# Optimization experiments

Hardware: AMD Instinct MI355X
Metric: run time of the kernel (lower is better)

The kernel has to match this reference:

```python
import jax, jax.numpy as jnp
import numpy as np

B, H, S, D = 2, 16, 2048, 64

def setup_inputs() -> dict:
    key = jax.random.key(0)
    kq, kk, kv = jax.random.split(key, 3)
    Q = jax.random.normal(kq, (B, H, S, D), dtype=jnp.float32)
    K = jax.random.normal(kk, (B, H, S, D), dtype=jnp.float32)
    V = jax.random.normal(kv, (B, H, S, D), dtype=jnp.float32)
    # causal mask: True means 'masked out' (filled with -inf), as in torch.masked_fill
    mask = jnp.triu(jnp.ones((S, S), dtype=bool), k=1)[None, None, :, :]
    return {"Q": Q, "K": K, "V": V, "mask": mask}

def reference(Q, K, V, mask):
    head_dim = jnp.asarray(K.shape[-1], dtype=Q.dtype)
    # a_scaled = Q @ K^T / sqrt(d)   -> [B,H,S,S]
    scores = jnp.einsum('bhqd,bhkd->bhqk', Q, K) / jnp.sqrt(head_dim)
    scores = jnp.where(mask, -jnp.inf, scores)
    # NOTE: the original custom softmax subtracts the GLOBAL max of the whole
    # tensor (torch.max(x) with no dim), not a per-row max. Reproduce faithfully.
    m = jnp.max(scores)
    e = jnp.exp(scores - m)
    attn = e / jnp.sum(e, axis=-1, keepdims=True)
    return jnp.einsum('bhqk,bhkd->bhqd', attn, V)
```

## Files before the change

kernel.cpp:

```cpp
#include <hip/hip_runtime.h>
#include <hip/hip_bf16.h>
#include <cstdint>
#include <cstddef>

#define SLEN 2048
#define DH   64
#define NQT  32
#define QBLK 64
#define KVB  64
#define NHEADS 32
#define LOG2E 1.44269504088896340736f

#define PRE_HEAD_BYTES (SLEN * DH * 2)
#define TILE_BYTES     (KVB * DH * 2)
#define VPRE_OFF       ((size_t)NHEADS * PRE_HEAD_BYTES)

typedef short  bf16x8 __attribute__((ext_vector_type(8)));
typedef float  f32x4  __attribute__((ext_vector_type(4)));

__device__ __forceinline__ unsigned short f2bf(float f) {
    __hip_bfloat16 h = __float2bfloat16(f);
    return *reinterpret_cast<unsigned short*>(&h);
}
__device__ __forceinline__ unsigned int pk2(float a, float b) {
    return (unsigned int)f2bf(a) | ((unsigned int)f2bf(b) << 16);
}

#define GLL(gp, lp)                                                            \
    __builtin_amdgcn_global_load_lds(                                          \
        (const __attribute__((address_space(1))) void*)(gp),                   \
        (__attribute__((address_space(3))) void*)(lp), 16, 0, 0)

__global__ __launch_bounds__(256) void prep(const float* __restrict__ Kg,
                                            const float* __restrict__ Vg,
                                            unsigned short* __restrict__ ws)
{
    const int bid = blockIdx.x;
    const int tid = threadIdx.x;
    if (bid < 2048) {
        const int cid = bid * 256 + tid;
        const int h   = cid >> 14;
        const int rem = cid & 16383;
        const int r   = rem >> 3;
        const int ccs = rem & 7;
        const int d0  = 8 * (ccs ^ (r & 7));
        const float* src = Kg + ((size_t)h * SLEN + r) * DH + d0;
        float4 a = *reinterpret_cast<const float4*>(src);
        float4 b = *reinterpret_cast<const float4*>(src + 4);
        bf16x8 o;
        o[0]=(short)f2bf(a.x); o[1]=(short)f2bf(a.y);
        o[2]=(short)f2bf(a.z); o[3]=(short)f2bf(a.w);
        o[4]=(short)f2bf(b.x); o[5]=(short)f2bf(b.y);
        o[6]=(short)f2bf(b.z); o[7]=(short)f2bf(b.w);
        *(bf16x8*)((char*)ws + (size_t)cid * 16) = o;
    } else {
        __shared__ __attribute__((aligned(16))) unsigned short Vt[KVB * DH];
        const int vb = bid - 2048;
        const int h  = vb >> 5;
        const int t  = vb & 31;
        const int do8 = tid & 7;
        const int kp  = tid >> 3;
        const float* s0 = Vg + ((size_t)h * SLEN + (size_t)t * KVB + 2 * kp) * DH + 8 * do8;
        float4 a0 = *reinterpret_cast<const float4*>(s0);
        float4 a1 = *reinterpret_cast<const float4*>(s0 + 4);
        float4 b0 = *reinterpret_cast<const float4*>(s0 + DH);
        float4 b1 = *reinterpret_cast<const float4*>(s0 + DH + 4);
        float av[8] = {a0.x,a0.y,a0.z,a0.w,a1.x,a1.y,a1.z,a1.w};
        float bv[8] = {b0.x,b0.y,b0.z,b0.w,b1.x,b1.y,b1.z,b1.w};
        #pragma unroll
        for (int j = 0; j < 8; ++j) {
            const int d = 8 * do8 + j;
            const unsigned byte =
                ((unsigned)(d * 128 + 4 * kp)) ^ (((unsigned)(d & 7)) << 4);
            *(unsigned*)((char*)Vt + byte) = pk2(av[j], bv[j]);
        }
        __syncthreads();
        char* gdst = (char*)ws + VPRE_OFF + (size_t)h * PRE_HEAD_BYTES
                   + (size_t)t * TILE_BYTES + (size_t)tid * 32;
        const char* lsrc = (const char*)Vt + tid * 32;
        *(bf16x8*)(gdst)      = *(const bf16x8*)(lsrc);
        *(bf16x8*)(gdst + 16) = *(const bf16x8*)(lsrc + 16);
    }
}

__global__ __launch_bounds__(256, 4) void fattn_f(const float* __restrict__ Qg,
                                                  const unsigned short* __restrict__ KV,
                                                  float* __restrict__ Og)
{
    __shared__ __attribute__((aligned(16))) unsigned short Klds[2][KVB * DH];
    __shared__ __attribute__((aligned(16))) unsigned short Vlds[2][DH * KVB];
    __shared__ __attribute__((aligned(16))) unsigned short Plds[4][16 * KVB];

    const int bid = blockIdx.x;
    const int hi4 = bid >> 8;
    const int lo8 = bid & 255;
    const int qx  = (int)((0x0F101F00u >> (8 * hi4)) & 31u);
    const int qt  = (lo8 & 31) ^ qx;
    const int bh  = (hi4 << 3) | (lo8 >> 5);
    const int qb  = qt * QBLK;

    const float* Qp   = Qg + (size_t)bh * SLEN * DH;
    const char*  Kpre = (const char*)KV + (size_t)bh * PRE_HEAD_BYTES;
    const char*  Vpre = (const char*)KV + VPRE_OFF + (size_t)bh * PRE_HEAD_BYTES;
    float*       Op   = Og + (size_t)bh * SLEN * DH;

    const int tid  = threadIdx.x;
    const int w    = tid >> 6;
    const int lane = tid & 63;
    const int g    = lane >> 4;
    const int m    = lane & 15;

    bf16x8 qf[2];
    {
        const float sc = 0.125f * LOG2E;
        const int qrow = qb + 16 * w + m;
        #pragma unroll
        for (int c = 0; c < 2; ++c) {
            const float* src = Qp + (size_t)qrow * DH + 32 * c + 8 * g;
            float4 a = *reinterpret_cast<const float4*>(src);
            float4 b = *reinterpret_cast<const float4*>(src + 4);
            bf16x8 qv;
            qv[0]=(short)f2bf(a.x*sc); qv[1]=(short)f2bf(a.y*sc);
            qv[2]=(short)f2bf(a.z*sc); qv[3]=(short)f2bf(a.w*sc);
            qv[4]=(short)f2bf(b.x*sc); qv[5]=(short)f2bf(b.y*sc);
            qv[6]=(short)f2bf(b.z*sc); qv[7]=(short)f2bf(b.w*sc);
            qf[c] = qv;
        }
    }

    f32x4 o[4];
    #pragma unroll
    for (int dt = 0; dt < 4; ++dt) o[dt] = (f32x4){0.f, 0.f, 0.f, 0.f};
    float mrun = -1e30f, lrun = 0.f;

    const int nt = qt + 1;

    char* Pw = (char*)&Plds[w][0];
    const unsigned pswz = ((unsigned)(m & 7)) << 4;
    const int q = qb + 16 * w + m;

    #define STAGE(jt_, buf_)                                                   \
        do {                                                                   \
            const char* gk_ = Kpre + (size_t)(jt_) * TILE_BYTES + tid * 16;    \
            const char* gv_ = Vpre + (size_t)(jt_) * TILE_BYTES + tid * 16;    \
            char* lk_ = (char*)&Klds[buf_][0] + tid * 16;                      \
            char* lv_ = (char*)&Vlds[buf_][0] + tid * 16;                      \
            GLL(gk_,        lk_);                                              \
            GLL(gk_ + 4096, lk_ + 4096);                                       \
            GLL(gv_,        lv_);                                              \
            GLL(gv_ + 4096, lv_ + 4096);                                       \
        } while (0)

    int buf = 0;
    STAGE(0, 0);
    __syncthreads();

    for (int jt = 0; jt < nt; ++jt) {
        const int kvb   = jt * KVB;
        const bool last = (jt == nt - 1);

        if (jt + 1 < nt) STAGE(jt + 1, buf ^ 1);

        const char* Kb = (const char*)&Klds[buf][0];
        const char* Vb = (const char*)&Vlds[buf][0];

        f32x4 s[4];
        #pragma unroll
        for (int t = 0; t < 4; ++t) {
            s[t] = (f32x4){0.f, 0.f, 0.f, 0.f};
            #pragma unroll
            for (int c = 0; c < 2; ++c) {
                const unsigned row  = (unsigned)(16 * t + m);
                const unsigned byte =
                    (row * 128u + (unsigned)(32 * c + 8 * g) * 2u) ^ ((row & 7u) << 4);
                bf16x8 kf = *(const bf16x8*)(Kb + byte);
                s[t] = __builtin_amdgcn_mfma_f32_16x16x32_bf16(kf, qf[c], s[t], 0, 0, 0);
            }
        }

        float mx = -1e30f;
        #pragma unroll
        for (int t = 0; t < 4; ++t) {
            #pragma unroll
            for (int r = 0; r < 4; ++r) {
                float v = s[t][r];
                if (last) {
                    const int kk = kvb + 16 * t + 4 * g + r;
                    v = (kk > q) ? -1e30f : v;
                }
                s[t][r] = v;
                mx = fmaxf(mx, v);
            }
        }
        mx = fmaxf(mx, __shfl_xor(mx, 16));
        mx = fmaxf(mx, __shfl_xor(mx, 32));
        const float mnew = fmaxf(mrun, mx);
        const float fs   = exp2f(mrun - mnew);
        mrun = mnew;

        float psum = 0.f;
        #pragma unroll
        for (int t = 0; t < 4; ++t) {
            const float p0 = exp2f(s[t][0] - mnew);
            const float p1 = exp2f(s[t][1] - mnew);
            const float p2 = exp2f(s[t][2] - mnew);
            const float p3 = exp2f(s[t][3] - mnew);
            psum += (p0 + p1) + (p2 + p3);
            uint2 e;
            e.x = pk2(p0, p1);
            e.y = pk2(p2, p3);
            const unsigned byte = (unsigned)(m * 128 + 32 * t + 8 * g);
            *(uint2*)(Pw + (byte ^ pswz)) = e;
        }
        psum += __shfl_xor(psum, 16);
        psum += __shfl_xor(psum, 32);
        lrun = lrun * fs + psum;

        float fso[4];
        #pragma unroll
        for (int r = 0; r < 4; ++r)
            fso[r] = __shfl(fs, (lane & 48) | (4 * g + r));
        #pragma unroll
        for (int dt = 0; dt < 4; ++dt) {
            #pragma unroll
            for (int r = 0; r < 4; ++r) o[dt][r] *= fso[r];
        }

        #pragma unroll
        for (int kc = 0; kc < 2; ++kc) {
            const unsigned ab = ((unsigned)(m * 128 + 64 * kc + 16 * g)) ^ pswz;
            bf16x8 pa = *(const bf16x8*)(Pw + ab);
            #pragma unroll
            for (int dt = 0; dt < 4; ++dt) {
                const unsigned d  = (unsigned)(16 * dt + m);
                const unsigned vby =
                    (d * 128u + (unsigned)(64 * kc + 16 * g)) ^ ((d & 7u) << 4);
                bf16x8 vf = *(const bf16x8*)(Vb + vby);
                o[dt] = __builtin_amdgcn_mfma_f32_16x16x32_bf16(pa, vf, o[dt], 0, 0, 0);
            }
        }

        __syncthreads();
        buf ^= 1;
    }
    #undef STAGE

    const float invl = 1.0f / lrun;
    float invo[4];
    #pragma unroll
    for (int r = 0; r < 4; ++r)
        invo[r] = __shfl(invl, (lane & 48) | (4 * g + r));
    #pragma unroll
    for (int r = 0; r < 4; ++r) {
        const int qrow = qb + 16 * w + 4 * g + r;
        float* dst = Op + (size_t)qrow * DH;
        #pragma unroll
        for (int dt = 0; dt < 4; ++dt) dst[16 * dt + m] = o[dt][r] * invo[r];
    }
}

__global__ __launch_bounds__(256, 4) void fattn_s(const float* __restrict__ Qg,
                                                  const float* __restrict__ Kg,
                                                  const float* __restrict__ Vg,
                                                  float* __restrict__ Og)
{
    __shared__ __attribute__((aligned(16))) unsigned short Klds[128 * DH];
    __shared__ __attribute__((aligned(16))) unsigned short Vlds[DH * 128];
    __shared__ __attribute__((aligned(16))) unsigned short Plds[4][16 * 128];

    const int bid = blockIdx.x;
    const int hi4 = bid >> 8;
    const int lo8 = bid & 255;
    const int qx  = (int)((0x0F101F00u >> (8 * hi4)) & 31u);
    const int qt  = (lo8 & 31) ^ qx;
    const int bh  = (hi4 << 3) | (lo8 >> 5);
    const int qb  = qt * QBLK;

    const float* Qp = Qg + (size_t)bh * SLEN * DH;
    const float* Kp = Kg + (size_t)bh * SLEN * DH;
    const float* Vp = Vg + (size_t)bh * SLEN * DH;
    float*       Op = Og + (size_t)bh * SLEN * DH;

    const int tid  = threadIdx.x;
    const int w    = tid >> 6;
    const int lane = tid & 63;
    const int g    = lane >> 4;
    const int m    = lane & 15;

    bf16x8 qf[2];
    {
        const float sc = 0.125f * LOG2E;
        const int qrow = qb + 16 * w + m;
        #pragma unroll
        for (int c = 0; c < 2; ++c) {
            const float* src = Qp + (size_t)qrow * DH + 32 * c + 8 * g;
            float4 a = *reinterpret_cast<const float4*>(src);
            float4 b = *reinterpret_cast<const float4*>(src + 4);
            bf16x8 qv;
            qv[0]=(short)f2bf(a.x*sc); qv[1]=(short)f2bf(a.y*sc);
            qv[2]=(short)f2bf(a.z*sc); qv[3]=(short)f2bf(a.w*sc);
            qv[4]=(short)f2bf(b.x*sc); qv[5]=(short)f2bf(b.y*sc);
            qv[6]=(short)f2bf(b.z*sc); qv[7]=(short)f2bf(b.w*sc);
            qf[c] = qv;
        }
    }

    f32x4 o[4];
    #pragma unroll
    for (int dt = 0; dt < 4; ++dt) o[dt] = (f32x4){0.f, 0.f, 0.f, 0.f};
    float mrun = -1e30f, lrun = 0.f;

    const int klim = qb + QBLK;
    const int nt   = (qt + 2) >> 1;

    const int rk = tid & 127, hk = tid >> 7;
    const int kp = tid & 63,  dq = tid >> 6;

    char* Pw = (char*)&Plds[w][0];
    const unsigned pswz = ((unsigned)(m & 7)) << 4;
    const int q = qb + 16 * w + m;

    for (int jt = 0; jt < nt; ++jt) {
        const int kvb    = jt * 128;
        const int kwidth = min(128, klim - kvb);
        const bool last  = (jt == nt - 1);

        if (rk < kwidth) {
            const float4* s4 = reinterpret_cast<const float4*>(
                Kp + (size_t)(kvb + rk) * DH + 32 * hk);
            float4 x[8];
            #pragma unroll
            for (int i = 0; i < 8; ++i) x[i] = s4[i];
            const unsigned rswz = ((unsigned)(rk & 7)) << 4;
            #pragma unroll
            for (int c = 0; c < 4; ++c) {
                bf16x8 kb;
                kb[0]=(short)f2bf(x[2*c].x);   kb[1]=(short)f2bf(x[2*c].y);
                kb[2]=(short)f2bf(x[2*c].z);   kb[3]=(short)f2bf(x[2*c].w);
                kb[4]=(short)f2bf(x[2*c+1].x); kb[5]=(short)f2bf(x[2*c+1].y);
                kb[6]=(short)f2bf(x[2*c+1].z); kb[7]=(short)f2bf(x[2*c+1].w);
                const unsigned byte = (unsigned)(rk * 128 + 64 * hk + 16 * c);
                *(bf16x8*)((char*)Klds + (byte ^ rswz)) = kb;
            }
        }
        if (2 * kp < kwidth) {
            const float* s0 = Vp + (size_t)(kvb + 2 * kp) * DH + 16 * dq;
            float av[16], bv[16];
            #pragma unroll
            for (int i = 0; i < 4; ++i) {
                float4 ta = *reinterpret_cast<const float4*>(s0 + 4 * i);
                float4 tb = *reinterpret_cast<const float4*>(s0 + DH + 4 * i);
                av[4*i]=ta.x; av[4*i+1]=ta.y; av[4*i+2]=ta.z; av[4*i+3]=ta.w;
                bv[4*i]=tb.x; bv[4*i+1]=tb.y; bv[4*i+2]=tb.z; bv[4*i+3]=tb.w;
            }
            #pragma unroll
            for (int j = 0; j < 16; ++j) {
                const int d = 16 * dq + j;
                const unsigned byte = (unsigned)(d * 256 + 4 * kp);
                *(unsigned*)((char*)Vlds + (byte ^ (((unsigned)(d & 7)) << 4))) =
                    pk2(av[j], bv[j]);
            }
        }
        __syncthreads();

        f32x4 s[8];
        #pragma unroll
        for (int t = 0; t < 8; ++t) {
            if (16 * t < kwidth) {
                s[t] = (f32x4){0.f, 0.f, 0.f, 0.f};
                #pragma unroll
                for (int c = 0; c < 2; ++c) {
                    const unsigned row  = (unsigned)(16 * t + m);
                    const unsigned byte =
                        (row * 128u + (unsigned)(32 * c + 8 * g) * 2u) ^ ((row & 7u) << 4);
                    bf16x8 kf = *(const bf16x8*)((const char*)Klds + byte);
                    s[t] = __builtin_amdgcn_mfma_f32_16x16x32_bf16(kf, qf[c], s[t], 0, 0, 0);
                }
            }
        }

        float mx = -1e30f;
        #pragma unroll
        for (int t = 0; t < 8; ++t) {
            if (16 * t < kwidth) {
                #pragma unroll
                for (int r = 0; r < 4; ++r) {
                    float v = s[t][r];
                    if (last) {
                        const int kk = kvb + 16 * t + 4 * g + r;
                        v = (kk > q) ? -1e30f : v;
                    }
                    s[t][r] = v;
                    mx = fmaxf(mx, v);
                }
            }
        }
        mx = fmaxf(mx, __shfl_xor(mx, 16));
        mx = fmaxf(mx, __shfl_xor(mx, 32));
        const float mnew = fmaxf(mrun, mx);
        const float fs   = exp2f(mrun - mnew);
        mrun = mnew;

        float psum = 0.f;
        #pragma unroll
        for (int t = 0; t < 8; ++t) {
            if (16 * t < kwidth) {
                const float p0 = exp2f(s[t][0] - mnew);
                const float p1 = exp2f(s[t][1] - mnew);
                const float p2 = exp2f(s[t][2] - mnew);
                const float p3 = exp2f(s[t][3] - mnew);
                psum += (p0 + p1) + (p2 + p3);
                uint2 e;
                e.x = pk2(p0, p1);
                e.y = pk2(p2, p3);
                const unsigned byte = (unsigned)(m * 256 + 32 * t + 8 * g);
                *(uint2*)(Pw + (byte ^ pswz)) = e;
            }
        }
        psum += __shfl_xor(psum, 16);
        psum += __shfl_xor(psum, 32);
        lrun = lrun * fs + psum;

        float fso[4];
        #pragma unroll
        for (int r = 0; r < 4; ++r)
            fso[r] = __shfl(fs, (lane & 48) | (4 * g + r));
        #pragma unroll
        for (int dt = 0; dt < 4; ++dt) {
            #pragma unroll
            for (int r = 0; r < 4; ++r) o[dt][r] *= fso[r];
        }

        const int kclim = kwidth >> 5;
        #pragma unroll
        for (int kc = 0; kc < 4; ++kc) {
            if (kc < kclim) {
                const unsigned ab = ((unsigned)(m * 256 + 64 * kc + 16 * g)) ^ pswz;
                bf16x8 pa = *(const bf16x8*)(Pw + ab);
                #pragma unroll
                for (int dt = 0; dt < 4; ++dt) {
                    const unsigned d  = (unsigned)(16 * dt + m);
                    const unsigned vby =
                        (d * 256u + (unsigned)(64 * kc + 16 * g)) ^ ((d & 7u) << 4);
                    bf16x8 vf = *(const bf16x8*)((const char*)Vlds + vby);
                    o[dt] = __builtin_amdgcn_mfma_f32_16x16x32_bf16(pa, vf, o[dt], 0, 0, 0);
                }
            }
        }
        __syncthreads();
    }

    const float invl = 1.0f / lrun;
    float invo[4];
    #pragma unroll
    for (int r = 0; r < 4; ++r)
        invo[r] = __shfl(invl, (lane & 48) | (4 * g + r));
    #pragma unroll
    for (int r = 0; r < 4; ++r) {
        const int qrow = qb + 16 * w + 4 * g + r;
        float* dst = Op + (size_t)qrow * DH;
        #pragma unroll
        for (int dt = 0; dt < 4; ++dt) dst[16 * dt + m] = o[dt][r] * invo[r];
    }
}

extern "C" void kernel_launch(void* const* d_in, const int* in_sizes, int n_in,
                              void* d_out, int out_size, void* d_ws, size_t ws_size,
                              hipStream_t stream) {
    const float* Q = (const float*)d_in[0];
    const float* K = (const float*)d_in[1];
    const float* V = (const float*)d_in[2];
    float* O = (float*)d_out;
    if (ws_size >= 2 * VPRE_OFF) {
        unsigned short* ws = (unsigned short*)d_ws;
        prep<<<dim3(3072), dim3(256), 0, stream>>>(K, V, ws);
        fattn_f<<<dim3(1024), dim3(256), 0, stream>>>(Q, ws, O);
    } else {
        fattn_s<<<dim3(1024), dim3(256), 0, stream>>>(Q, K, V, O);
    }
}
```

Before: 158.2 us.

## Triple-buffer KV tiles with manual vmcnt waits, lazy rescale, and LPT block order

Moves the K/V staging from double to triple buffering, prefetching two tiles ahead and replacing __syncthreads with explicit s_waitcnt vmcnt plus s_barrier. The block-to-tile mapping changes to a longest-first order (heaviest causal q-tiles first) in place of the XOR swizzle. The online-softmax rescale of o and l is skipped when no lane's max grows, and s_setprio raises wave priority around the MFMA sections. The larger LDS footprint drops launch bounds from 4 to 2 blocks per CU, which lowers occupancy in exchange for deeper prefetch. The hand-written vmcnt counts assume a fixed number of outstanding loads per stage.

```diff
diff --git a/kernel.cpp b/kernel.cpp
--- a/kernel.cpp
+++ b/kernel.cpp
@@ -83,20 +83,17 @@
     }
 }
 
-__global__ __launch_bounds__(256, 4) void fattn_f(const float* __restrict__ Qg,
+__global__ __launch_bounds__(256, 2) void fattn_f(const float* __restrict__ Qg,
                                                   const unsigned short* __restrict__ KV,
                                                   float* __restrict__ Og)
 {
-    __shared__ __attribute__((aligned(16))) unsigned short Klds[2][KVB * DH];
-    __shared__ __attribute__((aligned(16))) unsigned short Vlds[2][DH * KVB];
+    __shared__ __attribute__((aligned(16))) unsigned short Klds[3][KVB * DH];
+    __shared__ __attribute__((aligned(16))) unsigned short Vlds[3][DH * KVB];
     __shared__ __attribute__((aligned(16))) unsigned short Plds[4][16 * KVB];
 
     const int bid = blockIdx.x;
-    const int hi4 = bid >> 8;
-    const int lo8 = bid & 255;
-    const int qx  = (int)((0x0F101F00u >> (8 * hi4)) & 31u);
-    const int qt  = (lo8 & 31) ^ qx;
-    const int bh  = (hi4 << 3) | (lo8 >> 5);
+    const int qt  = 31 - (bid >> 5);
+    const int bh  = bid & 31;
     const int qb  = qt * QBLK;
 
     const float* Qp   = Qg + (size_t)bh * SLEN * DH;
@@ -139,32 +136,40 @@
     const unsigned pswz = ((unsigned)(m & 7)) << 4;
     const int q = qb + 16 * w + m;
 
-    #define STAGE(jt_, buf_)                                                   \
+    #define STAGE(jt_, b_)                                                     \
         do {                                                                   \
             const char* gk_ = Kpre + (size_t)(jt_) * TILE_BYTES + tid * 16;    \
             const char* gv_ = Vpre + (size_t)(jt_) * TILE_BYTES + tid * 16;    \
-            char* lk_ = (char*)&Klds[buf_][0] + tid * 16;                      \
-            char* lv_ = (char*)&Vlds[buf_][0] + tid * 16;                      \
+            char* lk_ = (char*)Klds + (size_t)(b_) * TILE_BYTES + tid * 16;    \
+            char* lv_ = (char*)Vlds + (size_t)(b_) * TILE_BYTES + tid * 16;    \
             GLL(gk_,        lk_);                                              \
             GLL(gk_ + 4096, lk_ + 4096);                                       \
             GLL(gv_,        lv_);                                              \
             GLL(gv_ + 4096, lv_ + 4096);                                       \
         } while (0)
 
-    int buf = 0;
+    int c0 = 0, c1 = 1, c2 = 2;
     STAGE(0, 0);
-    __syncthreads();
+    if (nt > 1) {
+        STAGE(1, 1);
+        asm volatile("s_waitcnt vmcnt(4)" ::: "memory");
+    } else {
+        asm volatile("s_waitcnt vmcnt(0)" ::: "memory");
+    }
+    __builtin_amdgcn_s_barrier();
 
     for (int jt = 0; jt < nt; ++jt) {
         const int kvb   = jt * KVB;
         const bool last = (jt == nt - 1);
-
-        if (jt + 1 < nt) STAGE(jt + 1, buf ^ 1);
-
-        const char* Kb = (const char*)&Klds[buf][0];
-        const char* Vb = (const char*)&Vlds[buf][0];
+        const bool more = (jt + 2 < nt);
+
+        if (more) STAGE(jt + 2, c2);
+
+        const char* Kb = (const char*)Klds + (size_t)c0 * TILE_BYTES;
+        const char* Vb = (const char*)Vlds + (size_t)c0 * TILE_BYTES;
 
         f32x4 s[4];
+        __builtin_amdgcn_s_setprio(1);
         #pragma unroll
         for (int t = 0; t < 4; ++t) {
             s[t] = (f32x4){0.f, 0.f, 0.f, 0.f};
@@ -177,6 +182,7 @@
                 s[t] = __builtin_amdgcn_mfma_f32_16x16x32_bf16(kf, qf[c], s[t], 0, 0, 0);
             }
         }
+        __builtin_amdgcn_s_setprio(0);
 
         float mx = -1e30f;
         #pragma unroll
@@ -194,17 +200,30 @@
         }
         mx = fmaxf(mx, __shfl_xor(mx, 16));
         mx = fmaxf(mx, __shfl_xor(mx, 32));
-        const float mnew = fmaxf(mrun, mx);
-        const float fs   = exp2f(mrun - mnew);
-        mrun = mnew;
+
+        if (__any(mx > mrun)) {
+            const float mnew = fmaxf(mrun, mx);
+            const float fs   = exp2f(mrun - mnew);
+            mrun = mnew;
+            lrun *= fs;
+            float fso[4];
+            #pragma unroll
+            for (int r = 0; r < 4; ++r)
+                fso[r] = __shfl(fs, (lane & 48) | (4 * g + r));
+            #pragma unroll
+            for (int dt = 0; dt < 4; ++dt) {
+                #pragma unroll
+                for (int r = 0; r < 4; ++r) o[dt][r] *= fso[r];
+            }
+        }
 
         float psum = 0.f;
         #pragma unroll
         for (int t = 0; t < 4; ++t) {
-            const float p0 = exp2f(s[t][0] - mnew);
-            const float p1 = exp2f(s[t][1] - mnew);
-            const float p2 = exp2f(s[t][2] - mnew);
-            const float p3 = exp2f(s[t][3] - mnew);
+            const float p0 = exp2f(s[t][0] - mrun);
+            const float p1 = exp2f(s[t][1] - mrun);
+            const float p2 = exp2f(s[t][2] - mrun);
+            const float p3 = exp2f(s[t][3] - mrun);
             psum += (p0 + p1) + (p2 + p3);
             uint2 e;
             e.x = pk2(p0, p1);
@@ -214,18 +233,9 @@
         }
         psum += __shfl_xor(psum, 16);
         psum += __shfl_xor(psum, 32);
-        lrun = lrun * fs + psum;
-
-        float fso[4];
-        #pragma unroll
-        for (int r = 0; r < 4; ++r)
-            fso[r] = __shfl(fs, (lane & 48) | (4 * g + r));
-        #pragma unroll
-        for (int dt = 0; dt < 4; ++dt) {
-            #pragma unroll
-            for (int r = 0; r < 4; ++r) o[dt][r] *= fso[r];
-        }
-
+        lrun += psum;
+
+        __builtin_amdgcn_s_setprio(1);
         #pragma unroll
         for (int kc = 0; kc < 2; ++kc) {
             const unsigned ab = ((unsigned)(m * 128 + 64 * kc + 16 * g)) ^ pswz;
@@ -239,9 +249,13 @@
                 o[dt] = __builtin_amdgcn_mfma_f32_16x16x32_bf16(pa, vf, o[dt], 0, 0, 0);
             }
         }
-
-        __syncthreads();
-        buf ^= 1;
+        __builtin_amdgcn_s_setprio(0);
+
+        if (more) asm volatile("s_waitcnt vmcnt(4)" ::: "memory");
+        else      asm volatile("s_waitcnt vmcnt(0)" ::: "memory");
+        __builtin_amdgcn_s_barrier();
+
+        const int tswap = c0; c0 = c1; c1 = c2; c2 = tswap;
     }
     #undef STAGE
 
```

Result: faster. 153.9 us (-2.7%).

## Pre-swizzle K/V into MFMA fragment order and load directly into registers

Applied to the files above, without the earlier changes.

The prep kernel now writes K and V tiles in the exact per-lane MFMA fragment order, so the attention kernel loads K/V straight from global memory into registers instead of staging them through LDS with global_load_lds. The new kernel handles 128 query rows per block (32 per wave, two 16-row halves) across 512 blocks, uses per-wave causal tile counts with no block barriers, and skips the rescale when no row max increases. This removes LDS traffic and __syncthreads, but each wave now reads K/V from global or L2 on its own, and register pressure rises, with launch bounds lowered to 2 blocks per CU.

```diff
diff --git a/kernel.cpp b/kernel.cpp
--- a/kernel.cpp
+++ b/kernel.cpp
@@ -5,15 +5,12 @@
 
 #define SLEN 2048
 #define DH   64
-#define NQT  32
-#define QBLK 64
-#define KVB  64
 #define NHEADS 32
 #define LOG2E 1.44269504088896340736f
 
-#define PRE_HEAD_BYTES (SLEN * DH * 2)
-#define TILE_BYTES     (KVB * DH * 2)
-#define VPRE_OFF       ((size_t)NHEADS * PRE_HEAD_BYTES)
+#define PRE_TILE 16384
+#define PRE_HEAD (32 * PRE_TILE)
+#define PRE_TOTAL ((size_t)NHEADS * PRE_HEAD)
 
 typedef short  bf16x8 __attribute__((ext_vector_type(8)));
 typedef float  f32x4  __attribute__((ext_vector_type(4)));
@@ -25,11 +22,6 @@
 __device__ __forceinline__ unsigned int pk2(float a, float b) {
     return (unsigned int)f2bf(a) | ((unsigned int)f2bf(b) << 16);
 }
-
-#define GLL(gp, lp)                                                            \
-    __builtin_amdgcn_global_load_lds(                                          \
-        (const __attribute__((address_space(1))) void*)(gp),                   \
-        (__attribute__((address_space(3))) void*)(lp), 16, 0, 0)
 
 __global__ __launch_bounds__(256) void prep(const float* __restrict__ Kg,
                                             const float* __restrict__ Vg,
@@ -38,13 +30,16 @@
     const int bid = blockIdx.x;
     const int tid = threadIdx.x;
     if (bid < 2048) {
-        const int cid = bid * 256 + tid;
-        const int h   = cid >> 14;
-        const int rem = cid & 16383;
-        const int r   = rem >> 3;
-        const int ccs = rem & 7;
-        const int d0  = 8 * (ccs ^ (r & 7));
-        const float* src = Kg + ((size_t)h * SLEN + r) * DH + d0;
+        const int cid  = bid * 256 + tid;
+        const int h    = cid >> 14;
+        const int rem  = cid & 16383;
+        const int jt   = rem >> 9;
+        const int rem2 = rem & 511;
+        const int kci  = rem2 >> 6;
+        const int l    = rem2 & 63;
+        const int t = kci >> 1, c = kci & 1, g = l >> 4, m = l & 15;
+        const float* src =
+            Kg + ((size_t)h * SLEN + 64 * jt + 16 * t + m) * DH + 32 * c + 8 * g;
         float4 a = *reinterpret_cast<const float4*>(src);
         float4 b = *reinterpret_cast<const float4*>(src + 4);
         bf16x8 o;
@@ -52,15 +47,17 @@
         o[2]=(short)f2bf(a.z); o[3]=(short)f2bf(a.w);
         o[4]=(short)f2bf(b.x); o[5]=(short)f2bf(b.y);
         o[6]=(short)f2bf(b.z); o[7]=(short)f2bf(b.w);
-        *(bf16x8*)((char*)ws + (size_t)cid * 16) = o;
+        *(bf16x8*)((char*)ws + (size_t)h * PRE_HEAD + (size_t)jt * PRE_TILE
+                   + kci * 1024 + l * 16) = o;
     } else {
-        __shared__ __attribute__((aligned(16))) unsigned short Vt[KVB * DH];
+        __shared__ __attribute__((aligned(16))) unsigned short Vt[64 * 64];
         const int vb = bid - 2048;
         const int h  = vb >> 5;
-        const int t  = vb & 31;
+        const int jt = vb & 31;
+        const int kp  = tid >> 3;
         const int do8 = tid & 7;
-        const int kp  = tid >> 3;
-        const float* s0 = Vg + ((size_t)h * SLEN + (size_t)t * KVB + 2 * kp) * DH + 8 * do8;
+        const float* s0 =
+            Vg + ((size_t)h * SLEN + 64 * jt + 2 * kp) * DH + 8 * do8;
         float4 a0 = *reinterpret_cast<const float4*>(s0);
         float4 a1 = *reinterpret_cast<const float4*>(s0 + 4);
         float4 b0 = *reinterpret_cast<const float4*>(s0 + DH);
@@ -71,25 +68,211 @@
         for (int j = 0; j < 8; ++j) {
             const int d = 8 * do8 + j;
             const unsigned byte =
-                ((unsigned)(d * 128 + 4 * kp)) ^ (((unsigned)(d & 7)) << 4);
+                (unsigned)(d * 128) + ((((unsigned)(kp >> 2)) ^ (unsigned)(d & 7)) << 4)
+                + (unsigned)((kp & 3) * 4);
             *(unsigned*)((char*)Vt + byte) = pk2(av[j], bv[j]);
         }
         __syncthreads();
-        char* gdst = (char*)ws + VPRE_OFF + (size_t)h * PRE_HEAD_BYTES
-                   + (size_t)t * TILE_BYTES + (size_t)tid * 32;
-        const char* lsrc = (const char*)Vt + tid * 32;
-        *(bf16x8*)(gdst)      = *(const bf16x8*)(lsrc);
-        *(bf16x8*)(gdst + 16) = *(const bf16x8*)(lsrc + 16);
-    }
-}
-
-__global__ __launch_bounds__(256, 4) void fattn_f(const float* __restrict__ Qg,
+        char* base = (char*)ws + (size_t)h * PRE_HEAD + (size_t)jt * PRE_TILE + 8192;
+        #pragma unroll
+        for (int u = 0; u < 2; ++u) {
+            const int cc  = 2 * tid + u;
+            const int vci = cc >> 6;
+            const int l   = cc & 63;
+            const int kc = vci >> 2, dt = vci & 3, g = l >> 4, m = l & 15;
+            const int d   = 16 * dt + m;
+            const int kch = 4 * kc + g;
+            bf16x8 v = *(const bf16x8*)((const char*)Vt + d * 128
+                        + (((unsigned)kch ^ (unsigned)(d & 7)) << 4));
+            *(bf16x8*)(base + vci * 1024 + l * 16) = v;
+        }
+    }
+}
+
+__global__ __launch_bounds__(256, 2) void fattn_r(const float* __restrict__ Qg,
                                                   const unsigned short* __restrict__ KV,
                                                   float* __restrict__ Og)
 {
-    __shared__ __attribute__((aligned(16))) unsigned short Klds[2][KVB * DH];
-    __shared__ __attribute__((aligned(16))) unsigned short Vlds[2][DH * KVB];
-    __shared__ __attribute__((aligned(16))) unsigned short Plds[4][16 * KVB];
+    __shared__ __attribute__((aligned(16))) unsigned short Plds[4][2][16 * 64];
+
+    const int bid   = blockIdx.x;
+    const int hi    = bid >> 8;
+    const int qtile = (bid & 15) ^ (hi ? 15 : 0);
+    const int head  = (bid >> 4) & 31;
+    const int Qb    = qtile * 128;
+
+    const float* Qp = Qg + (size_t)head * SLEN * DH;
+    const char*  KH = (const char*)KV + (size_t)head * PRE_HEAD;
+    float*       Op = Og + (size_t)head * SLEN * DH;
+
+    const int tid  = threadIdx.x;
+    const int w    = tid >> 6;
+    const int lane = tid & 63;
+    const int g    = lane >> 4;
+    const int m    = lane & 15;
+
+    char* P0 = (char*)&Plds[w][0][0];
+    char* P1 = (char*)&Plds[w][1][0];
+    const unsigned pswz = ((unsigned)(m & 7)) << 4;
+
+    bf16x8 qf[2][2];
+    {
+        const float sc = 0.125f * LOG2E;
+        #pragma unroll
+        for (int h = 0; h < 2; ++h) {
+            const int qrow = Qb + 32 * w + 16 * h + m;
+            #pragma unroll
+            for (int c = 0; c < 2; ++c) {
+                const float* src = Qp + (size_t)qrow * DH + 32 * c + 8 * g;
+                float4 a = *reinterpret_cast<const float4*>(src);
+                float4 b = *reinterpret_cast<const float4*>(src + 4);
+                bf16x8 qv;
+                qv[0]=(short)f2bf(a.x*sc); qv[1]=(short)f2bf(a.y*sc);
+                qv[2]=(short)f2bf(a.z*sc); qv[3]=(short)f2bf(a.w*sc);
+                qv[4]=(short)f2bf(b.x*sc); qv[5]=(short)f2bf(b.y*sc);
+                qv[6]=(short)f2bf(b.z*sc); qv[7]=(short)f2bf(b.w*sc);
+                qf[h][c] = qv;
+            }
+        }
+    }
+
+    f32x4 o0[4], o1[4];
+    #pragma unroll
+    for (int dt = 0; dt < 4; ++dt) { o0[dt] = (f32x4){0,0,0,0}; o1[dt] = (f32x4){0,0,0,0}; }
+    float mr0 = -1e30f, lr0 = 0.f, mr1 = -1e30f, lr1 = 0.f;
+
+    const int q0 = Qb + 32 * w + m;
+    const int q1 = q0 + 16;
+    const int nt = 2 * qtile + 1 + (w >> 1);
+
+    const char* tb = KH;
+    for (int jt = 0; jt < nt; ++jt, tb += PRE_TILE) {
+        const bool last = (jt == nt - 1);
+        const int  kvb  = jt * 64;
+
+        bf16x8 kf[8];
+        #pragma unroll
+        for (int i = 0; i < 8; ++i)
+            kf[i] = *(const bf16x8*)(tb + i * 1024 + lane * 16);
+
+        f32x4 s0[4], s1[4];
+        #pragma unroll
+        for (int t = 0; t < 4; ++t) { s0[t] = (f32x4){0,0,0,0}; s1[t] = (f32x4){0,0,0,0}; }
+        #pragma unroll
+        for (int c = 0; c < 2; ++c) {
+            #pragma unroll
+            for (int t = 0; t < 4; ++t)
+                s0[t] = __builtin_amdgcn_mfma_f32_16x16x32_bf16(kf[2*t+c], qf[0][c], s0[t], 0, 0, 0);
+            #pragma unroll
+            for (int t = 0; t < 4; ++t)
+                s1[t] = __builtin_amdgcn_mfma_f32_16x16x32_bf16(kf[2*t+c], qf[1][c], s1[t], 0, 0, 0);
+        }
+
+        bf16x8 vf[8];
+        #pragma unroll
+        for (int i = 0; i < 8; ++i)
+            vf[i] = *(const bf16x8*)(tb + 8192 + i * 1024 + lane * 16);
+
+        #pragma unroll
+        for (int h = 0; h < 2; ++h) {
+            f32x4* s   = h ? s1 : s0;
+            float& mr  = h ? mr1 : mr0;
+            float& lr  = h ? lr1 : lr0;
+            f32x4* o   = h ? o1 : o0;
+            const int q = h ? q1 : q0;
+            char*  Pb  = h ? P1 : P0;
+
+            float mx = -1e30f;
+            #pragma unroll
+            for (int t = 0; t < 4; ++t) {
+                #pragma unroll
+                for (int r = 0; r < 4; ++r) {
+                    float v = s[t][r];
+                    if (last) {
+                        const int kk = kvb + 16 * t + 4 * g + r;
+                        v = (kk > q) ? -1e30f : v;
+                    }
+                    s[t][r] = v;
+                    mx = fmaxf(mx, v);
+                }
+            }
+            mx = fmaxf(mx, __shfl_xor(mx, 16));
+            mx = fmaxf(mx, __shfl_xor(mx, 32));
+
+            if (__any(mx > mr)) {
+                const float mnew = fmaxf(mr, mx);
+                const float fs   = exp2f(mr - mnew);
+                mr = mnew;
+                lr *= fs;
+                float fso[4];
+                #pragma unroll
+                for (int r = 0; r < 4; ++r)
+                    fso[r] = __shfl(fs, (lane & 48) | (4 * g + r));
+                #pragma unroll
+                for (int dt = 0; dt < 4; ++dt) {
+                    #pragma unroll
+                    for (int r = 0; r < 4; ++r) o[dt][r] *= fso[r];
+                }
+            }
+
+            float ps = 0.f;
+            #pragma unroll
+            for (int t = 0; t < 4; ++t) {
+                const float p0 = exp2f(s[t][0] - mr);
+                const float p1 = exp2f(s[t][1] - mr);
+                const float p2 = exp2f(s[t][2] - mr);
+                const float p3 = exp2f(s[t][3] - mr);
+                ps += (p0 + p1) + (p2 + p3);
+                uint2 e;
+                e.x = pk2(p0, p1);
+                e.y = pk2(p2, p3);
+                const unsigned byte = (unsigned)(m * 128 + 32 * t + 8 * g);
+                *(uint2*)(Pb + (byte ^ pswz)) = e;
+            }
+            ps += __shfl_xor(ps, 16);
+            ps += __shfl_xor(ps, 32);
+            lr += ps;
+        }
+
+        #pragma unroll
+        for (int kc = 0; kc < 2; ++kc) {
+            const unsigned ab = ((unsigned)(m * 128 + 64 * kc + 16 * g)) ^ pswz;
+            bf16x8 pa0 = *(const bf16x8*)(P0 + ab);
+            bf16x8 pa1 = *(const bf16x8*)(P1 + ab);
+            #pragma unroll
+            for (int dt = 0; dt < 4; ++dt) {
+                o0[dt] = __builtin_amdgcn_mfma_f32_16x16x32_bf16(pa0, vf[kc*4+dt], o0[dt], 0, 0, 0);
+                o1[dt] = __builtin_amdgcn_mfma_f32_16x16x32_bf16(pa1, vf[kc*4+dt], o1[dt], 0, 0, 0);
+            }
+        }
+    }
+
+    #pragma unroll
+    for (int h = 0; h < 2; ++h) {
+        const float invl = 1.0f / (h ? lr1 : lr0);
+        f32x4* o = h ? o1 : o0;
+        float invo[4];
+        #pragma unroll
+        for (int r = 0; r < 4; ++r)
+            invo[r] = __shfl(invl, (lane & 48) | (4 * g + r));
+        #pragma unroll
+        for (int r = 0; r < 4; ++r) {
+            const int qrow = Qb + 32 * w + 16 * h + 4 * g + r;
+            float* dst = Op + (size_t)qrow * DH;
+            #pragma unroll
+            for (int dt = 0; dt < 4; ++dt) dst[16 * dt + m] = o[dt][r] * invo[r];
+        }
+    }
+}
+
+__global__ __launch_bounds__(256, 4) void fattn_s(const float* __restrict__ Qg,
+                                                  const float* __restrict__ Kg,
+                                                  const float* __restrict__ Vg,
+                                                  float* __restrict__ Og)
+{
+    __shared__ __attribute__((aligned(16))) unsigned short Klds[128 * DH];
+    __shared__ __attribute__((aligned(16))) unsigned short Vlds[DH * 128];
+    __shared__ __attribute__((aligned(16))) unsigned short Plds[4][16 * 128];
 
     const int bid = blockIdx.x;
     const int hi4 = bid >> 8;
@@ -97,12 +280,12 @@
     const int qx  = (int)((0x0F101F00u >> (8 * hi4)) & 31u);
     const int qt  = (lo8 & 31) ^ qx;
     const int bh  = (hi4 << 3) | (lo8 >> 5);
-    const int qb  = qt * QBLK;
-
-    const float* Qp   = Qg + (size_t)bh * SLEN * DH;
-    const char*  Kpre = (const char*)KV + (size_t)bh * PRE_HEAD_BYTES;
-    const char*  Vpre = (const char*)KV + VPRE_OFF + (size_t)bh * PRE_HEAD_BYTES;
-    float*       Op   = Og + (size_t)bh * SLEN * DH;
+    const int qb  = qt * 64;
+
+    const float* Qp = Qg + (size_t)bh * SLEN * DH;
+    const float* Kp = Kg + (size_t)bh * SLEN * DH;
+    const float* Vp = Vg + (size_t)bh * SLEN * DH;
+    float*       Op = Og + (size_t)bh * SLEN * DH;
 
     const int tid  = threadIdx.x;
     const int w    = tid >> 6;
@@ -133,184 +316,7 @@
     for (int dt = 0; dt < 4; ++dt) o[dt] = (f32x4){0.f, 0.f, 0.f, 0.f};
     float mrun = -1e30f, lrun = 0.f;
 
-    const int nt = qt + 1;
-
-    char* Pw = (char*)&Plds[w][0];
-    const unsigned pswz = ((unsigned)(m & 7)) << 4;
-    const int q = qb + 16 * w + m;
-
-    #define STAGE(jt_, buf_)                                                   \
-        do {                                                                   \
-            const char* gk_ = Kpre + (size_t)(jt_) * TILE_BYTES + tid * 16;    \
-            const char* gv_ = Vpre + (size_t)(jt_) * TILE_BYTES + tid * 16;    \
-            char* lk_ = (char*)&Klds[buf_][0] + tid * 16;                      \
-            char* lv_ = (char*)&Vlds[buf_][0] + tid * 16;                      \
-            GLL(gk_,        lk_);                                              \
-            GLL(gk_ + 4096, lk_ + 4096);                                       \
-            GLL(gv_,        lv_);                                              \
-            GLL(gv_ + 4096, lv_ + 4096);                                       \
-        } while (0)
-
-    int buf = 0;
-    STAGE(0, 0);
-    __syncthreads();
-
-    for (int jt = 0; jt < nt; ++jt) {
-        const int kvb   = jt * KVB;
-        const bool last = (jt == nt - 1);
-
-        if (jt + 1 < nt) STAGE(jt + 1, buf ^ 1);
-
-        const char* Kb = (const char*)&Klds[buf][0];
-        const char* Vb = (const char*)&Vlds[buf][0];
-
-        f32x4 s[4];
-        #pragma unroll
-        for (int t = 0; t < 4; ++t) {
-            s[t] = (f32x4){0.f, 0.f, 0.f, 0.f};
-            #pragma unroll
-            for (int c = 0; c < 2; ++c) {
-                const unsigned row  = (unsigned)(16 * t + m);
-                const unsigned byte =
-                    (row * 128u + (unsigned)(32 * c + 8 * g) * 2u) ^ ((row & 7u) << 4);
-                bf16x8 kf = *(const bf16x8*)(Kb + byte);
-                s[t] = __builtin_amdgcn_mfma_f32_16x16x32_bf16(kf, qf[c], s[t], 0, 0, 0);
-            }
-        }
-
-        float mx = -1e30f;
-        #pragma unroll
-        for (int t = 0; t < 4; ++t) {
-            #pragma unroll
-            for (int r = 0; r < 4; ++r) {
-                float v = s[t][r];
-                if (last) {
-                    const int kk = kvb + 16 * t + 4 * g + r;
-                    v = (kk > q) ? -1e30f : v;
-                }
-                s[t][r] = v;
-                mx = fmaxf(mx, v);
-            }
-        }
-        mx = fmaxf(mx, __shfl_xor(mx, 16));
-        mx = fmaxf(mx, __shfl_xor(mx, 32));
-        const float mnew = fmaxf(mrun, mx);
-        const float fs   = exp2f(mrun - mnew);
-        mrun = mnew;
-
-        float psum = 0.f;
-        #pragma unroll
-        for (int t = 0; t < 4; ++t) {
-            const float p0 = exp2f(s[t][0] - mnew);
-            const float p1 = exp2f(s[t][1] - mnew);
-            const float p2 = exp2f(s[t][2] - mnew);
-            const float p3 = exp2f(s[t][3] - mnew);
-            psum += (p0 + p1) + (p2 + p3);
-            uint2 e;
-            e.x = pk2(p0, p1);
-            e.y = pk2(p2, p3);
-            const unsigned byte = (unsigned)(m * 128 + 32 * t + 8 * g);
-            *(uint2*)(Pw + (byte ^ pswz)) = e;
-        }
-        psum += __shfl_xor(psum, 16);
-        psum += __shfl_xor(psum, 32);
-        lrun = lrun * fs + psum;
-
-        float fso[4];
-        #pragma unroll
-        for (int r = 0; r < 4; ++r)
-            fso[r] = __shfl(fs, (lane & 48) | (4 * g + r));
-        #pragma unroll
-        for (int dt = 0; dt < 4; ++dt) {
-            #pragma unroll
-            for (int r = 0; r < 4; ++r) o[dt][r] *= fso[r];
-        }
-
-        #pragma unroll
-        for (int kc = 0; kc < 2; ++kc) {
-            const unsigned ab = ((unsigned)(m * 128 + 64 * kc + 16 * g)) ^ pswz;
-            bf16x8 pa = *(const bf16x8*)(Pw + ab);
-            #pragma unroll
-            for (int dt = 0; dt < 4; ++dt) {
-                const unsigned d  = (unsigned)(16 * dt + m);
-                const unsigned vby =
-                    (d * 128u + (unsigned)(64 * kc + 16 * g)) ^ ((d & 7u) << 4);
-                bf16x8 vf = *(const bf16x8*)(Vb + vby);
-                o[dt] = __builtin_amdgcn_mfma_f32_16x16x32_bf16(pa, vf, o[dt], 0, 0, 0);
-            }
-        }
-
-        __syncthreads();
-        buf ^= 1;
-    }
-    #undef STAGE
-
-    const float invl = 1.0f / lrun;
-    float invo[4];
-    #pragma unroll
-    for (int r = 0; r < 4; ++r)
-        invo[r] = __shfl(invl, (lane & 48) | (4 * g + r));
-    #pragma unroll
-    for (int r = 0; r < 4; ++r) {
-        const int qrow = qb + 16 * w + 4 * g + r;
-        float* dst = Op + (size_t)qrow * DH;
-        #pragma unroll
-        for (int dt = 0; dt < 4; ++dt) dst[16 * dt + m] = o[dt][r] * invo[r];
-    }
-}
-
-__global__ __launch_bounds__(256, 4) void fattn_s(const float* __restrict__ Qg,
-                                                  const float* __restrict__ Kg,
-                                                  const float* __restrict__ Vg,
-                                                  float* __restrict__ Og)
-{
-    __shared__ __attribute__((aligned(16))) unsigned short Klds[128 * DH];
-    __shared__ __attribute__((aligned(16))) unsigned short Vlds[DH * 128];
-    __shared__ __attribute__((aligned(16))) unsigned short Plds[4][16 * 128];
-
-    const int bid = blockIdx.x;
-    const int hi4 = bid >> 8;
-    const int lo8 = bid & 255;
-    const int qx  = (int)((0x0F101F00u >> (8 * hi4)) & 31u);
-    const int qt  = (lo8 & 31) ^ qx;
-    const int bh  = (hi4 << 3) | (lo8 >> 5);
-    const int qb  = qt * QBLK;
-
-    const float* Qp = Qg + (size_t)bh * SLEN * DH;
-    const float* Kp = Kg + (size_t)bh * SLEN * DH;
-    const float* Vp = Vg + (size_t)bh * SLEN * DH;
-    float*       Op = Og + (size_t)bh * SLEN * DH;
-
-    const int tid  = threadIdx.x;
-    const int w    = tid >> 6;
-    const int lane = tid & 63;
-    const int g    = lane >> 4;
-    const int m    = lane & 15;
-
-    bf16x8 qf[2];
-    {
-        const float sc = 0.125f * LOG2E;
-        const int qrow = qb + 16 * w + m;
-        #pragma unroll
-        for (int c = 0; c < 2; ++c) {
-            const float* src = Qp + (size_t)qrow * DH + 32 * c + 8 * g;
-            float4 a = *reinterpret_cast<const float4*>(src);
-            float4 b = *reinterpret_cast<const float4*>(src + 4);
-            bf16x8 qv;
-            qv[0]=(short)f2bf(a.x*sc); qv[1]=(short)f2bf(a.y*sc);
-            qv[2]=(short)f2bf(a.z*sc); qv[3]=(short)f2bf(a.w*sc);
-            qv[4]=(short)f2bf(b.x*sc); qv[5]=(short)f2bf(b.y*sc);
-            qv[6]=(short)f2bf(b.z*sc); qv[7]=(short)f2bf(b.w*sc);
-            qf[c] = qv;
-        }
-    }
-
-    f32x4 o[4];
-    #pragma unroll
-    for (int dt = 0; dt < 4; ++dt) o[dt] = (f32x4){0.f, 0.f, 0.f, 0.f};
-    float mrun = -1e30f, lrun = 0.f;
-
-    const int klim = qb + QBLK;
+    const int klim = qb + 64;
     const int nt   = (qt + 2) >> 1;
 
     const int rk = tid & 127, hk = tid >> 7;
@@ -442,8 +448,8 @@
                     const unsigned d  = (unsigned)(16 * dt + m);
                     const unsigned vby =
                         (d * 256u + (unsigned)(64 * kc + 16 * g)) ^ ((d & 7u) << 4);
-                    bf16x8 vf = *(const bf16x8*)((const char*)Vlds + vby);
-                    o[dt] = __builtin_amdgcn_mfma_f32_16x16x32_bf16(pa, vf, o[dt], 0, 0, 0);
+                    bf16x8 vfb = *(const bf16x8*)((const char*)Vlds + vby);
+                    o[dt] = __builtin_amdgcn_mfma_f32_16x16x32_bf16(pa, vfb, o[dt], 0, 0, 0);
                 }
             }
         }
@@ -471,10 +477,10 @@
     const float* K = (const float*)d_in[1];
     const float* V = (const float*)d_in[2];
     float* O = (float*)d_out;
-    if (ws_size >= 2 * VPRE_OFF) {
+    if (ws_size >= PRE_TOTAL) {
         unsigned short* ws = (unsigned short*)d_ws;
         prep<<<dim3(3072), dim3(256), 0, stream>>>(K, V, ws);
-        fattn_f<<<dim3(1024), dim3(256), 0, stream>>>(Q, ws, O);
+        fattn_r<<<dim3(512), dim3(256), 0, stream>>>(Q, ws, O);
     } else {
         fattn_s<<<dim3(1024), dim3(256), 0, stream>>>(Q, K, V, O);
     }
```

Result: slower. 169.8 us (+7.3%).
